# Kernel tuning notes

Hardware: AMD Instinct MI355X
Metric: run time of the kernel (lower is better)

Reference implementation:

```python
import jax, jax.numpy as jnp
import numpy as np

B, H, W, N = 4, 64, 64, 64
NEAR, FAR = 2.0, 6.0
HID = 64


def setup_inputs() -> dict:
    key = jax.random.key(0)
    ks = jax.random.split(key, 6)
    ray_origins = jnp.tile(jnp.array([0.0, 0.0, 4.0], jnp.float32), (B, H, W, 1))
    ray_directions = jax.random.normal(ks[0], (B, H, W, 3), jnp.float32)
    tform_cam2world = jnp.eye(4, dtype=jnp.float32) + 0.1 * jax.random.normal(ks[1], (B, 4, 4), jnp.float32)
    depth_noise = jax.random.uniform(ks[2], (B, H, W, N), jnp.float32)
    u_samples = jax.random.uniform(ks[3], (B, H, W, N), jnp.float32)
    W1 = 0.5 * jax.random.normal(ks[4], (3, HID), jnp.float32)
    b1 = jnp.zeros((HID,), jnp.float32)
    W2 = 0.5 * jax.random.normal(ks[5], (HID, 4), jnp.float32)
    b2 = jnp.zeros((4,), jnp.float32)
    return dict(ray_origins=ray_origins, ray_directions=ray_directions,
                tform_cam2world=tform_cam2world, depth_noise=depth_noise,
                u_samples=u_samples, W1=W1, b1=b1, W2=W2, b2=b2)


def field(pts, W1, b1, W2, b2):
    # tiny radiance-field MLP standing in for the generator's sampler
    h = jax.nn.relu(pts @ W1 + b1)
    out = h @ W2 + b2
    sigma = out[..., 0]
    rgb = jax.nn.sigmoid(out[..., 1:4])
    return sigma, rgb


def compositing_weights(sigma, z_vals):
    # alpha-compositing weights (render_volume_density)
    dists = jnp.concatenate([z_vals[..., 1:] - z_vals[..., :-1],
                             jnp.full_like(z_vals[..., :1], 1e10)], axis=-1)
    alpha = 1.0 - jnp.exp(-jax.nn.relu(sigma) * dists)
    trans = jnp.cumprod(1.0 - alpha + 1e-10, axis=-1)
    trans = jnp.concatenate([jnp.ones_like(trans[..., :1]), trans[..., :-1]], axis=-1)
    return alpha * trans


def sample_pdf(bins, weights, u):
    # bins [R, M+1], weights [R, M], u [R, S] -> samples [R, S]
    pdf = weights / jnp.sum(weights, axis=-1, keepdims=True)
    cdf = jnp.cumsum(pdf, axis=-1)
    cdf = jnp.concatenate([jnp.zeros_like(cdf[..., :1]), cdf], axis=-1)  # [R, M+1]
    inds = jax.vmap(lambda c, uu: jnp.searchsorted(c, uu, side='right'))(cdf, u)
    last = cdf.shape[-1] - 1
    below = jnp.clip(inds - 1, 0, last)
    above = jnp.clip(inds, 0, last)
    cdf_b = jnp.take_along_axis(cdf, below, axis=-1)
    cdf_a = jnp.take_along_axis(cdf, above, axis=-1)
    bin_b = jnp.take_along_axis(bins, below, axis=-1)
    bin_a = jnp.take_along_axis(bins, above, axis=-1)
    denom = cdf_a - cdf_b
    denom = jnp.where(denom < 1e-5, 1.0, denom)
    t = (u - cdf_b) / denom
    return bin_b + t * (bin_a - bin_b)


def reference(ray_origins, ray_directions, tform_cam2world, depth_noise, u_samples, W1, b1, W2, b2):
    rd = ray_directions / jnp.linalg.norm(ray_directions, axis=-1, keepdims=True)
    # stratified coarse samples along each ray
    t = (jnp.arange(N, dtype=jnp.float32) + depth_noise) / N           # [B,H,W,N]
    z_vals = NEAR + (FAR - NEAR) * t
    pts = ray_origins[..., None, :] + rd[..., None, :] * z_vals[..., None]
    sigma, rgb = field(pts, W1, b1, W2, b2)                            # [B,H,W,N], [B,H,W,N,3]

    # --- hierarchical importance sampling (no_grad in original) ---
    w = compositing_weights(sigma, z_vals).reshape(-1, N)              # [R,N]
    pad = jnp.pad(w, ((0, 0), (1, 1)), constant_values=-jnp.inf)
    mx = jnp.maximum(pad[:, :-1], pad[:, 1:])                          # max_pool1d(k=2,s=1,p=1) -> [R,N+1]
    sm = 0.5 * (mx[:, :-1] + mx[:, 1:]) + 0.01                        # avg_pool1d(k=2,s=1)  -> [R,N]
    z_mid = (0.5 * (z_vals[..., 1:] + z_vals[..., :-1])).reshape(-1, N - 1)
    z_samples = sample_pdf(z_mid, sm[:, 1:-1], u_samples.reshape(-1, N))
    z_samples = jax.lax.stop_gradient(z_samples.reshape(B, H, W, N))

    # fine evaluation + merge-sort of coarse/fine samples
    z_all = jnp.concatenate([z_vals, z_samples], axis=-1)              # [B,H,W,2N]
    idx = jnp.argsort(z_all, axis=-1)
    z_sorted = jnp.take_along_axis(z_all, idx, axis=-1)
    pts_f = ray_origins[..., None, :] + rd[..., None, :] * z_samples[..., None]
    sigma_f, rgb_f = field(pts_f, W1, b1, W2, b2)
    sigma_all = jnp.take_along_axis(jnp.concatenate([sigma, sigma_f], axis=-1), idx, axis=-1)
    rgb_cat = jnp.concatenate([rgb, rgb_f], axis=-2)
    rgb_all = jnp.take_along_axis(rgb_cat, jnp.broadcast_to(idx[..., None], idx.shape + (3,)), axis=-2)

    # final alpha compositing
    w_all = compositing_weights(sigma_all, z_sorted)
    rgb_pred = jnp.sum(w_all[..., None] * rgb_all, axis=-2)            # [B,H,W,3]
    depth_pred = jnp.sum(w_all * z_sorted, axis=-1)                    # [B,H,W]
    mask_pred = jnp.sum(w_all, axis=-1)                                # [B,H,W]

    # camera-space depth (invert_space: R_w2c = R^T)
    R_w2c = jnp.swapaxes(tform_cam2world[:, :3, :3], -1, -2)           # [B,3,3]
    view_dir = jnp.einsum('bhwj,bij->bhwi', rd, R_w2c)
    depth_cam = -(view_dir * depth_pred[..., None])[..., -1]
    return rgb_pred, depth_cam, mask_pred
```

## Files before the change

kernel.cpp:

```cpp
#include <hip/hip_runtime.h>
#include <hip/hip_bf16.h>
#include <math.h>

#define Nn    64
#define RPB   2
#define NRAYS 16384
#define NEARV 2.0f
#define FARV  6.0f

typedef __attribute__((ext_vector_type(8))) short bf16x8;
typedef __attribute__((ext_vector_type(4))) float f32x4;
typedef __attribute__((ext_vector_type(2))) float f32x2;

template <int CTRL, int RMASK>
__device__ __forceinline__ float dpp_mv(float x, float ident) {
  return __int_as_float(__builtin_amdgcn_update_dpp(
      __float_as_int(ident), __float_as_int(x), CTRL, RMASK, 0xf, false));
}
template <int CTRL, int RMASK>
__device__ __forceinline__ int dpp_mvi(int x, int ident) {
  return __builtin_amdgcn_update_dpp(ident, x, CTRL, RMASK, 0xf, false);
}
__device__ __forceinline__ float shfl_up1(float x) {
  return __int_as_float(__builtin_amdgcn_update_dpp(
      __float_as_int(x), __float_as_int(x), 0x138, 0xf, 0xf, false));
}
__device__ __forceinline__ float shfl_dn1(float x) {
  return __int_as_float(__builtin_amdgcn_update_dpp(
      __float_as_int(x), __float_as_int(x), 0x130, 0xf, 0xf, false));
}
__device__ __forceinline__ float scan_add_dpp(float x) {
  x += dpp_mv<0x111, 0xf>(x, 0.f);
  x += dpp_mv<0x112, 0xf>(x, 0.f);
  x += dpp_mv<0x114, 0xf>(x, 0.f);
  x += dpp_mv<0x118, 0xf>(x, 0.f);
  x += dpp_mv<0x142, 0xa>(x, 0.f);
  x += dpp_mv<0x143, 0xc>(x, 0.f);
  return x;
}
__device__ __forceinline__ int scan_add_dpp_int(int x) {
  x += dpp_mvi<0x111, 0xf>(x, 0);
  x += dpp_mvi<0x112, 0xf>(x, 0);
  x += dpp_mvi<0x114, 0xf>(x, 0);
  x += dpp_mvi<0x118, 0xf>(x, 0);
  x += dpp_mvi<0x142, 0xa>(x, 0);
  x += dpp_mvi<0x143, 0xc>(x, 0);
  return x;
}
__device__ __forceinline__ float scan_mul_dpp(float x) {
  x *= dpp_mv<0x111, 0xf>(x, 1.f);
  x *= dpp_mv<0x112, 0xf>(x, 1.f);
  x *= dpp_mv<0x114, 0xf>(x, 1.f);
  x *= dpp_mv<0x118, 0xf>(x, 1.f);
  x *= dpp_mv<0x142, 0xa>(x, 1.f);
  x *= dpp_mv<0x143, 0xc>(x, 1.f);
  return x;
}
__device__ __forceinline__ float reduce_add_bcast(float x) {
  x = scan_add_dpp(x);
  return __int_as_float(__builtin_amdgcn_readlane(__float_as_int(x), 63));
}

__device__ __forceinline__ float fast_rcp(float x) { return __builtin_amdgcn_rcpf(x); }
__device__ __forceinline__ float sigmoidf_fast(float x) { return fast_rcp(1.f + __expf(-x)); }

__device__ __forceinline__ short bfhi_bits(float x) { return (short)(__float_as_uint(x) >> 16); }
__device__ __forceinline__ float bfhi_val(float x)  { return __uint_as_float(__float_as_uint(x) & 0xFFFF0000u); }

template <int LEVEL, int D>
__device__ __forceinline__ void bitonic_stage(unsigned& k, int lane) {
  unsigned t;
  if constexpr (D == 32) {
    t = (unsigned)__builtin_amdgcn_ds_bpermute((lane ^ 32) << 2, (int)k);
  } else {
    t = (unsigned)__builtin_amdgcn_ds_swizzle((int)k, (D << 10) | 0x1F);
  }
  const bool bitd = (lane & D) != 0;
  const bool desc = (lane & (1 << LEVEL)) != 0;
  const unsigned mn = (k < t) ? k : t;
  const unsigned mx = (k < t) ? t : k;
  k = (bitd == desc) ? mn : mx;
}
template <int LEVEL, int D>
struct BSort {
  static __device__ __forceinline__ void run(unsigned& k, int lane) {
    bitonic_stage<LEVEL, D>(k, lane);
    if constexpr (D > 1) BSort<LEVEL, D / 2>::run(k, lane);
    else if constexpr (LEVEL < 6) BSort<LEVEL + 1, (1 << LEVEL)>::run(k, lane);
  }
};

__device__ __forceinline__ int count_le_f(float arr, float x) {
  int cnt = 0;
#pragma unroll
  for (int step = 32; step >= 1; step >>= 1) {
    const int idx = cnt + step - 1;
    const float v = __shfl(arr, idx, 64);
    if (idx < 63 && v <= x) cnt += step;
  }
  return cnt;
}

template <bool SPLITB>
__device__ __forceinline__ void field_eval(
    float zlane, const f32x2 c0v[2][4], const f32x2 c1v[2][4],
    const bf16x8 aHi[2], const bf16x8 aLo[2],
    float b20, float b21, float b22, float b23,
    int quad, int col, float4* scratch, float o[4]) {
#pragma unroll
  for (int nt = 0; nt < 4; ++nt) {
    f32x4 acc = {0.f, 0.f, 0.f, 0.f};
    const float zm = __shfl(zlane, nt * 16 + col, 64);
    const f32x2 zm2 = {zm, zm};
#pragma unroll
    for (int ks = 0; ks < 2; ++ks) {
      union { bf16x8 v; unsigned u[4]; } Bhi, Blo;
#pragma unroll
      for (int p = 0; p < 4; ++p) {
        f32x2 h = zm2 * c1v[ks][p] + c0v[ks][p];
        h = __builtin_elementwise_max(h, (f32x2){0.f, 0.f});
        if constexpr (SPLITB) {
          union { f32x2 f; unsigned u[2]; } U; U.f = h;
          Bhi.u[p] = __builtin_amdgcn_perm(U.u[1], U.u[0], 0x07060302u);
          union { unsigned u[2]; f32x2 f; } M;
          M.u[0] = U.u[0] & 0xFFFF0000u;
          M.u[1] = U.u[1] & 0xFFFF0000u;
          const f32x2 l = h - M.f;
          union { f32x2 f; unsigned u[2]; } L; L.f = l;
          Blo.u[p] = __builtin_amdgcn_perm(L.u[1], L.u[0], 0x07060302u);
        } else {
          __hip_bfloat162 t = __float22bfloat162_rn(make_float2(h[0], h[1]));
          Bhi.u[p] = *reinterpret_cast<unsigned*>(&t);
        }
      }
      if constexpr (SPLITB) {
        acc = __builtin_amdgcn_mfma_f32_16x16x32_bf16(aHi[ks], Bhi.v, acc, 0, 0, 0);
        acc = __builtin_amdgcn_mfma_f32_16x16x32_bf16(aHi[ks], Blo.v, acc, 0, 0, 0);
        acc = __builtin_amdgcn_mfma_f32_16x16x32_bf16(aLo[ks], Bhi.v, acc, 0, 0, 0);
      } else {
        acc = __builtin_amdgcn_mfma_f32_16x16x32_bf16(aHi[ks], Bhi.v, acc, 0, 0, 0);
        acc = __builtin_amdgcn_mfma_f32_16x16x32_bf16(aLo[ks], Bhi.v, acc, 0, 0, 0);
      }
    }
    if (quad == 0) scratch[nt * 16 + col] = make_float4(acc[0], acc[1], acc[2], acc[3]);
  }
  const float4 r = scratch[(threadIdx.x & 63)];
  o[0] = r.x + b20; o[1] = r.y + b21; o[2] = r.z + b22; o[3] = r.w + b23;
}

__global__ __launch_bounds__(RPB * 64, 5) void nerf_fused(
    const float* __restrict__ ray_o, const float* __restrict__ ray_d,
    const float* __restrict__ tform, const float* __restrict__ noise,
    const float* __restrict__ usmp,  const float* __restrict__ W1,
    const float* __restrict__ b1,    const float* __restrict__ W2,
    const float* __restrict__ b2,    float* __restrict__ out) {
  const int wave = threadIdx.x >> 6;
  const int lane = threadIdx.x & 63;
  const int ray  = blockIdx.x * RPB + wave;
  const int quad = lane >> 4;
  const int col  = lane & 15;

  __shared__ float2   sC  [RPB][Nn];
  __shared__ float4   sPk [RPB][2 * Nn];
  __shared__ unsigned sKey[RPB][2 * Nn];
  __shared__ unsigned sHist[RPB][Nn];

  sHist[wave][lane] = 0u;

  const float o0 = ray_o[ray * 3 + 0], o1 = ray_o[ray * 3 + 1], o2 = ray_o[ray * 3 + 2];
  float d0 = ray_d[ray * 3 + 0], d1 = ray_d[ray * 3 + 1], d2 = ray_d[ray * 3 + 2];
  const float rn = __builtin_amdgcn_rsqf(d0 * d0 + d1 * d1 + d2 * d2);
  d0 *= rn; d1 *= rn; d2 *= rn;

  {
    const float w10 = W1[lane], w11 = W1[64 + lane], w12 = W1[128 + lane];
    const float c1 = d0 * w10 + d1 * w11 + d2 * w12;
    const float c0 = o0 * w10 + o1 * w11 + o2 * w12 + b1[lane];
    sC[wave][lane] = make_float2(c0, c1);
  }

  const float nz = noise[ray * Nn + lane];
  const float z  = NEARV + (FARV - NEARV) * ((float)lane + nz) * (1.0f / Nn);
  const unsigned kc = ((__float_as_uint(z) - 0x40000000u) << 7) | (unsigned)lane;

  unsigned ub = __float_as_uint(usmp[ray * Nn + lane]);
  BSort<1, 1>::run(ub, lane);
  const float us = __uint_as_float(ub);

  f32x2 c0v[2][4], c1v[2][4];
#pragma unroll
  for (int ks = 0; ks < 2; ++ks) {
    const float4* cc4 = (const float4*)&sC[wave][0];
    const int base4 = (ks * 32 + quad * 8) >> 1;
#pragma unroll
    for (int jj = 0; jj < 4; ++jj) {
      const float4 v = cc4[base4 + jj];
      c0v[ks][jj] = (f32x2){v.x, v.z};
      c1v[ks][jj] = (f32x2){v.y, v.w};
    }
  }

  bf16x8 aHi[2], aLo[2];
#pragma unroll
  for (int ks = 0; ks < 2; ++ks) {
#pragma unroll
    for (int j = 0; j < 8; ++j) {
      const int k = ks * 32 + quad * 8 + j;
      const float wv  = (col < 4) ? W2[k * 4 + col] : 0.f;
      aHi[ks][j] = bfhi_bits(wv);
      aLo[ks][j] = bfhi_bits(wv - bfhi_val(wv));
    }
  }
  const float b20 = b2[0], b21 = b2[1], b22 = b2[2], b23 = b2[3];
  float4* scratch = &sPk[wave][64];

  float oc[4];
  field_eval<true>(z, c0v, c1v, aHi, aLo, b20, b21, b22, b23, quad, col, scratch, oc);
  const float sig = oc[0];
  const float cr = sigmoidf_fast(oc[1]), cg = sigmoidf_fast(oc[2]), cb = sigmoidf_fast(oc[3]);
  sPk[wave][lane] = make_float4(sig, cr, cg, cb);

  const float zn   = shfl_dn1(z);
  const float dist = (lane == 63) ? 1e10f : (zn - z);
  const float alpha = 1.f - __expf(-fmaxf(sig, 0.f) * dist);
  float cdfreg, binreg;
  {
    const float P  = scan_mul_dpp(1.f - alpha + 1e-10f);
    float Te = shfl_up1(P);
    if (lane == 0) Te = 1.f;
    const float w = alpha * Te;

    const float mxA = fmaxf(shfl_up1(w), w);
    const float mxB = fmaxf(w, shfl_dn1(w));
    const float sm = 0.5f * (mxA + mxB) + 0.01f;

    const float v   = (lane >= 1 && lane <= 62) ? sm : 0.f;
    const float tot = reduce_add_bcast(v);
    const float pdf = v * fast_rcp(tot);
    const float C   = scan_add_dpp(pdf);
    cdfreg = (lane == 0) ? 0.f : C;
    binreg = 0.5f * (z + zn);
  }

  const int lo_i = count_le_f(cdfreg, us);
  const int below = lo_i - 1;
  const int above = (lo_i < 63) ? lo_i : 62;
  const float cdfb = __shfl(cdfreg, below, 64);
  const float cdfa = __shfl(cdfreg, above, 64);
  const float binb = __shfl(binreg, below, 64);
  const float bina = __shfl(binreg, above, 64);
  float den = cdfa - cdfb;
  if (den < 1e-5f) den = 1.f;
  const float zs = fmaf((us - cdfb) * fast_rcp(den), bina - binb, binb);

  const float zb1 = __shfl(z, below + 1, 64);
  const int   cj  = below + 1 + ((zb1 <= zs) ? 1 : 0);
  const int   pos_f = lane + cj;
  const unsigned kf = ((__float_as_uint(zs) - 0x40000000u) << 7) | (unsigned)(64 + lane);

  atomicAdd(&sHist[wave][cj], 1u);

  float of[4];
  field_eval<false>(zs, c0v, c1v, aHi, aLo, b20, b21, b22, b23, quad, col, scratch, of);

  const int h    = (int)sHist[wave][lane];
  const int pref = scan_add_dpp_int(h);
  const int pos_c = lane + pref;

  const float sigF = of[0];
  const float fr = sigmoidf_fast(of[1]), fg = sigmoidf_fast(of[2]), fb = sigmoidf_fast(of[3]);
  sPk[wave][64 + lane] = make_float4(sigF, fr, fg, fb);

  sKey[wave][pos_c] = kc;
  sKey[wave][pos_f] = kf;
  const uint2 kk = *reinterpret_cast<const uint2*>(&sKey[wave][2 * lane]);
  const unsigned k0 = kk.x;
  const unsigned k1 = kk.y;

  const float z0 = __uint_as_float((k0 >> 7) + 0x40000000u);
  const float z1 = __uint_as_float((k1 >> 7) + 0x40000000u);
  const float4 q0 = sPk[wave][k0 & 127u];
  const float4 q1 = sPk[wave][k1 & 127u];

  const float z2 = shfl_dn1(z0);
  const float dist0 = z1 - z0;
  const float dist1 = (lane == 63) ? 1e10f : (z2 - z1);
  const float al0 = 1.f - __expf(-fmaxf(q0.x, 0.f) * dist0);
  const float al1 = 1.f - __expf(-fmaxf(q1.x, 0.f) * dist1);
  const float aa0 = 1.f - al0 + 1e-10f;
  const float aa1 = 1.f - al1 + 1e-10f;
  const float Pp = scan_mul_dpp(aa0 * aa1);
  float Tp = shfl_up1(Pp);
  if (lane == 0) Tp = 1.f;
  const float w0 = al0 * Tp;
  const float w1 = al1 * Tp * aa0;

  const float accR = reduce_add_bcast(w0 * q0.y + w1 * q1.y);
  const float accG = reduce_add_bcast(w0 * q0.z + w1 * q1.z);
  const float accB = reduce_add_bcast(w0 * q0.w + w1 * q1.w);
  const float accD = reduce_add_bcast(w0 * z0 + w1 * z1);
  const float accM = reduce_add_bcast(w0 + w1);

  if (lane == 0) {
    const float* tf = tform + (ray >> 12) * 16;
    const float vz = d0 * tf[2] + d1 * tf[6] + d2 * tf[10];
    out[ray * 3 + 0]     = accR;
    out[ray * 3 + 1]     = accG;
    out[ray * 3 + 2]     = accB;
    out[NRAYS * 3 + ray] = -vz * accD;
    out[NRAYS * 4 + ray] = accM;
  }
}

extern "C" void kernel_launch(void* const* d_in, const int* in_sizes, int n_in,
                              void* d_out, int out_size, void* d_ws, size_t ws_size,
                              hipStream_t stream) {
  const float* ray_o = (const float*)d_in[0];
  const float* ray_d = (const float*)d_in[1];
  const float* tform = (const float*)d_in[2];
  const float* noise = (const float*)d_in[3];
  const float* usmp  = (const float*)d_in[4];
  const float* W1    = (const float*)d_in[5];
  const float* b1    = (const float*)d_in[6];
  const float* W2    = (const float*)d_in[7];
  const float* b2    = (const float*)d_in[8];
  float* out = (float*)d_out;

  nerf_fused<<<dim3(NRAYS / RPB), RPB * 64, 0, stream>>>(
      ray_o, ray_d, tform, noise, usmp, W1, b1, W2, b2, out);
}
```

Measured before the change: 100.7 us.

## Replace per-sample MLP MFMA evaluation with piecewise-linear breakpoint scan

Along each ray the field MLP is a sum of ReLU hinges in z, so the output is piecewise linear with breakpoints at each hidden unit's zero crossing. Each hidden unit now finds where its hinge falls among the sorted sample depths and atomically scatters its slope and intercept contributions into per-sample LDS bins. Prefix scans over those bins then give exact linear coefficients for every sample, replacing the bf16 split MFMA evaluation for both coarse and fine passes. This trades MFMA work and bf16 error compensation for LDS float atomics, which may contend, plus extra wave scans. Float atomic ordering also makes the summation order nondeterministic.

```diff
diff --git a/kernel.cpp b/kernel.cpp
--- a/kernel.cpp
+++ b/kernel.cpp
@@ -1,5 +1,4 @@
 #include <hip/hip_runtime.h>
-#include <hip/hip_bf16.h>
 #include <math.h>
 
 #define Nn    64
@@ -7,10 +6,6 @@
 #define NRAYS 16384
 #define NEARV 2.0f
 #define FARV  6.0f
-
-typedef __attribute__((ext_vector_type(8))) short bf16x8;
-typedef __attribute__((ext_vector_type(4))) float f32x4;
-typedef __attribute__((ext_vector_type(2))) float f32x2;
 
 template <int CTRL, int RMASK>
 __device__ __forceinline__ float dpp_mv(float x, float ident) {
@@ -64,9 +59,6 @@
 __device__ __forceinline__ float fast_rcp(float x) { return __builtin_amdgcn_rcpf(x); }
 __device__ __forceinline__ float sigmoidf_fast(float x) { return fast_rcp(1.f + __expf(-x)); }
 
-__device__ __forceinline__ short bfhi_bits(float x) { return (short)(__float_as_uint(x) >> 16); }
-__device__ __forceinline__ float bfhi_val(float x)  { return __uint_as_float(__float_as_uint(x) & 0xFFFF0000u); }
-
 template <int LEVEL, int D>
 __device__ __forceinline__ void bitonic_stage(unsigned& k, int lane) {
   unsigned t;
@@ -101,51 +93,16 @@
   return cnt;
 }
 
-template <bool SPLITB>
-__device__ __forceinline__ void field_eval(
-    float zlane, const f32x2 c0v[2][4], const f32x2 c1v[2][4],
-    const bf16x8 aHi[2], const bf16x8 aLo[2],
-    float b20, float b21, float b22, float b23,
-    int quad, int col, float4* scratch, float o[4]) {
-#pragma unroll
-  for (int nt = 0; nt < 4; ++nt) {
-    f32x4 acc = {0.f, 0.f, 0.f, 0.f};
-    const float zm = __shfl(zlane, nt * 16 + col, 64);
-    const f32x2 zm2 = {zm, zm};
-#pragma unroll
-    for (int ks = 0; ks < 2; ++ks) {
-      union { bf16x8 v; unsigned u[4]; } Bhi, Blo;
-#pragma unroll
-      for (int p = 0; p < 4; ++p) {
-        f32x2 h = zm2 * c1v[ks][p] + c0v[ks][p];
-        h = __builtin_elementwise_max(h, (f32x2){0.f, 0.f});
-        if constexpr (SPLITB) {
-          union { f32x2 f; unsigned u[2]; } U; U.f = h;
-          Bhi.u[p] = __builtin_amdgcn_perm(U.u[1], U.u[0], 0x07060302u);
-          union { unsigned u[2]; f32x2 f; } M;
-          M.u[0] = U.u[0] & 0xFFFF0000u;
-          M.u[1] = U.u[1] & 0xFFFF0000u;
-          const f32x2 l = h - M.f;
-          union { f32x2 f; unsigned u[2]; } L; L.f = l;
-          Blo.u[p] = __builtin_amdgcn_perm(L.u[1], L.u[0], 0x07060302u);
-        } else {
-          __hip_bfloat162 t = __float22bfloat162_rn(make_float2(h[0], h[1]));
-          Bhi.u[p] = *reinterpret_cast<unsigned*>(&t);
-        }
-      }
-      if constexpr (SPLITB) {
-        acc = __builtin_amdgcn_mfma_f32_16x16x32_bf16(aHi[ks], Bhi.v, acc, 0, 0, 0);
-        acc = __builtin_amdgcn_mfma_f32_16x16x32_bf16(aHi[ks], Blo.v, acc, 0, 0, 0);
-        acc = __builtin_amdgcn_mfma_f32_16x16x32_bf16(aLo[ks], Bhi.v, acc, 0, 0, 0);
-      } else {
-        acc = __builtin_amdgcn_mfma_f32_16x16x32_bf16(aHi[ks], Bhi.v, acc, 0, 0, 0);
-        acc = __builtin_amdgcn_mfma_f32_16x16x32_bf16(aLo[ks], Bhi.v, acc, 0, 0, 0);
-      }
-    }
-    if (quad == 0) scratch[nt * 16 + col] = make_float4(acc[0], acc[1], acc[2], acc[3]);
-  }
-  const float4 r = scratch[(threadIdx.x & 63)];
-  o[0] = r.x + b20; o[1] = r.y + b21; o[2] = r.z + b22; o[3] = r.w + b23;
+__device__ __forceinline__ int count_lt_sorted(float arr, float x) {
+  const float v63 = __shfl(arr, 63, 64);
+  int cnt = 0;
+#pragma unroll
+  for (int step = 32; step >= 1; step >>= 1) {
+    const int idx = cnt + step - 1;
+    const float v = __shfl(arr, idx, 64);
+    if (idx < 63 && v < x) cnt += step;
+  }
+  return (v63 < x) ? 64 : cnt;
 }
 
 __global__ __launch_bounds__(RPB * 64, 5) void nerf_fused(
@@ -157,27 +114,34 @@
   const int wave = threadIdx.x >> 6;
   const int lane = threadIdx.x & 63;
   const int ray  = blockIdx.x * RPB + wave;
-  const int quad = lane >> 4;
-  const int col  = lane & 15;
-
-  __shared__ float2   sC  [RPB][Nn];
+
+  __shared__ float    sP  [RPB][2][Nn][8];
   __shared__ float4   sPk [RPB][2 * Nn];
   __shared__ unsigned sKey[RPB][2 * Nn];
   __shared__ unsigned sHist[RPB][Nn];
 
   sHist[wave][lane] = 0u;
+  {
+    float4* zp = (float4*)&sP[wave][0][0][0];
+    const float4 z4 = make_float4(0.f, 0.f, 0.f, 0.f);
+    zp[lane] = z4; zp[64 + lane] = z4; zp[128 + lane] = z4; zp[192 + lane] = z4;
+  }
 
   const float o0 = ray_o[ray * 3 + 0], o1 = ray_o[ray * 3 + 1], o2 = ray_o[ray * 3 + 2];
   float d0 = ray_d[ray * 3 + 0], d1 = ray_d[ray * 3 + 1], d2 = ray_d[ray * 3 + 2];
   const float rn = __builtin_amdgcn_rsqf(d0 * d0 + d1 * d1 + d2 * d2);
   d0 *= rn; d1 *= rn; d2 *= rn;
 
-  {
-    const float w10 = W1[lane], w11 = W1[64 + lane], w12 = W1[128 + lane];
-    const float c1 = d0 * w10 + d1 * w11 + d2 * w12;
-    const float c0 = o0 * w10 + o1 * w11 + o2 * w12 + b1[lane];
-    sC[wave][lane] = make_float2(c0, c1);
-  }
+  const float w10 = W1[lane], w11 = W1[64 + lane], w12 = W1[128 + lane];
+  const float c1k = d0 * w10 + d1 * w11 + d2 * w12;
+  const float c0k = o0 * w10 + o1 * w11 + o2 * w12 + b1[lane];
+
+  const float4 w2r = *reinterpret_cast<const float4*>(W2 + lane * 4);
+  float g[8];
+  g[0] = w2r.x * c0k; g[1] = w2r.x * c1k;
+  g[2] = w2r.y * c0k; g[3] = w2r.y * c1k;
+  g[4] = w2r.z * c0k; g[5] = w2r.z * c1k;
+  g[6] = w2r.w * c0k; g[7] = w2r.w * c1k;
 
   const float nz = noise[ray * Nn + lane];
   const float z  = NEARV + (FARV - NEARV) * ((float)lane + nz) * (1.0f / Nn);
@@ -187,37 +151,59 @@
   BSort<1, 1>::run(ub, lane);
   const float us = __uint_as_float(ub);
 
-  f32x2 c0v[2][4], c1v[2][4];
-#pragma unroll
-  for (int ks = 0; ks < 2; ++ks) {
-    const float4* cc4 = (const float4*)&sC[wave][0];
-    const int base4 = (ks * 32 + quad * 8) >> 1;
-#pragma unroll
-    for (int jj = 0; jj < 4; ++jj) {
-      const float4 v = cc4[base4 + jj];
-      c0v[ks][jj] = (f32x2){v.x, v.z};
-      c1v[ks][jj] = (f32x2){v.y, v.w};
+  const float b20 = b2[0], b21 = b2[1], b22 = b2[2], b23 = b2[3];
+
+  const float zstar = -c0k * fast_rcp(c1k);
+
+  int sk_c;
+  {
+    const float tt = (zstar - NEARV) * 16.0f;
+    if (!(tt > 0.0f)) sk_c = 0;
+    else if (tt >= 64.0f) sk_c = 64;
+    else {
+      const int f = (int)tt;
+      const float nf = __shfl(nz, f, 64);
+      sk_c = f + (((float)f + nf < tt) ? 1 : 0);
     }
   }
 
-  bf16x8 aHi[2], aLo[2];
-#pragma unroll
-  for (int ks = 0; ks < 2; ++ks) {
-#pragma unroll
-    for (int j = 0; j < 8; ++j) {
-      const int k = ks * 32 + quad * 8 + j;
-      const float wv  = (col < 4) ? W2[k * 4 + col] : 0.f;
-      aHi[ks][j] = bfhi_bits(wv);
-      aLo[ks][j] = bfhi_bits(wv - bfhi_val(wv));
+  {
+    float* baseC = &sP[wave][0][0][0];
+    if (c1k > 0.0f) {
+      if (sk_c < 64) {
+        float* p = baseC + sk_c * 8;
+#pragma unroll
+        for (int j = 0; j < 8; ++j) atomicAdd(p + j, g[j]);
+      }
+    } else if (c1k < 0.0f) {
+      if (sk_c > 0) {
+#pragma unroll
+        for (int j = 0; j < 8; ++j) atomicAdd(baseC + j, g[j]);
+        if (sk_c < 64) {
+          float* p = baseC + sk_c * 8;
+#pragma unroll
+          for (int j = 0; j < 8; ++j) atomicAdd(p + j, -g[j]);
+        }
+      }
+    } else if (c0k > 0.0f) {
+#pragma unroll
+      for (int j = 0; j < 8; ++j) atomicAdd(baseC + j, g[j]);
     }
   }
-  const float b20 = b2[0], b21 = b2[1], b22 = b2[2], b23 = b2[3];
-  float4* scratch = &sPk[wave][64];
-
-  float oc[4];
-  field_eval<true>(z, c0v, c1v, aHi, aLo, b20, b21, b22, b23, quad, col, scratch, oc);
-  const float sig = oc[0];
-  const float cr = sigmoidf_fast(oc[1]), cg = sigmoidf_fast(oc[2]), cb = sigmoidf_fast(oc[3]);
+
+  float sig, cr, cg, cb;
+  {
+    const float4 pa = *reinterpret_cast<const float4*>(&sP[wave][0][lane][0]);
+    const float4 pb = *reinterpret_cast<const float4*>(&sP[wave][0][lane][4]);
+    const float P00 = scan_add_dpp(pa.x), P10 = scan_add_dpp(pa.y);
+    const float P01 = scan_add_dpp(pa.z), P11 = scan_add_dpp(pa.w);
+    const float P02 = scan_add_dpp(pb.x), P12 = scan_add_dpp(pb.y);
+    const float P03 = scan_add_dpp(pb.z), P13 = scan_add_dpp(pb.w);
+    sig = fmaf(z, P10, P00) + b20;
+    cr  = sigmoidf_fast(fmaf(z, P11, P01) + b21);
+    cg  = sigmoidf_fast(fmaf(z, P12, P02) + b22);
+    cb  = sigmoidf_fast(fmaf(z, P13, P03) + b23);
+  }
   sPk[wave][lane] = make_float4(sig, cr, cg, cb);
 
   const float zn   = shfl_dn1(z);
@@ -260,15 +246,49 @@
 
   atomicAdd(&sHist[wave][cj], 1u);
 
-  float of[4];
-  field_eval<false>(zs, c0v, c1v, aHi, aLo, b20, b21, b22, b23, quad, col, scratch, of);
+  const int sk_f = count_lt_sorted(zs, zstar);
+
+  {
+    float* baseF = &sP[wave][1][0][0];
+    if (c1k > 0.0f) {
+      if (sk_f < 64) {
+        float* p = baseF + sk_f * 8;
+#pragma unroll
+        for (int j = 0; j < 8; ++j) atomicAdd(p + j, g[j]);
+      }
+    } else if (c1k < 0.0f) {
+      if (sk_f > 0) {
+#pragma unroll
+        for (int j = 0; j < 8; ++j) atomicAdd(baseF + j, g[j]);
+        if (sk_f < 64) {
+          float* p = baseF + sk_f * 8;
+#pragma unroll
+          for (int j = 0; j < 8; ++j) atomicAdd(p + j, -g[j]);
+        }
+      }
+    } else if (c0k > 0.0f) {
+#pragma unroll
+      for (int j = 0; j < 8; ++j) atomicAdd(baseF + j, g[j]);
+    }
+  }
 
   const int h    = (int)sHist[wave][lane];
   const int pref = scan_add_dpp_int(h);
   const int pos_c = lane + pref;
 
-  const float sigF = of[0];
-  const float fr = sigmoidf_fast(of[1]), fg = sigmoidf_fast(of[2]), fb = sigmoidf_fast(of[3]);
+  float sigF, fr, fg, fb;
+  {
+    const float4 pa = *reinterpret_cast<const float4*>(&sP[wave][1][lane][0]);
+    const float4 pb = *reinterpret_cast<const float4*>(&sP[wave][1][lane][4]);
+    const float P00 = scan_add_dpp(pa.x), P10 = scan_add_dpp(pa.y);
+    const float P01 = scan_add_dpp(pa.z), P11 = scan_add_dpp(pa.w);
+    const float P02 = scan_add_dpp(pb.x), P12 = scan_add_dpp(pb.y);
+    const float P03 = scan_add_dpp(pb.z), P13 = scan_add_dpp(pb.w);
+    sigF = fmaf(zs, P10, P00) + b20;
+    fr   = sigmoidf_fast(fmaf(zs, P11, P01) + b21);
+    fg   = sigmoidf_fast(fmaf(zs, P12, P02) + b22);
+    fb   = sigmoidf_fast(fmaf(zs, P13, P03) + b23);
+  }
   sPk[wave][64 + lane] = make_float4(sigF, fr, fg, fb);
 
   sKey[wave][pos_c] = kc;
```

New measurement: 161.9 us. +60.8%, slower.
